# Kernel optimization log

Hardware: AMD Instinct MI355X
Metric: run time of the kernel (lower is better)

The kernel has to match this reference:

```python
import jax, jax.numpy as jnp
import numpy as np

HEADS = 8
DIM_HEAD = 64

def setup_inputs() -> dict:
    key = jax.random.key(0)
    ks = jax.random.split(key, 5)
    B, N, D = 2, 4096, 512  # query_dim = inner_dim = 512
    s = 0.02
    return {
        "x": jax.random.normal(ks[0], (B, N, D), dtype=jnp.float32),
        "Wq": jax.random.normal(ks[1], (D, D), dtype=jnp.float32) * s,
        "Wk": jax.random.normal(ks[2], (D, D), dtype=jnp.float32) * s,
        "Wv": jax.random.normal(ks[3], (D, D), dtype=jnp.float32) * s,
        "Wo": jax.random.normal(ks[4], (D, D), dtype=jnp.float32) * s,
        "bo": jnp.zeros((D,), dtype=jnp.float32),
    }

def reference(x, Wq, Wk, Wv, Wo, bo):
    B, N, D = x.shape
    h, dh = HEADS, DIM_HEAD
    scale = dh ** (-0.5)
    # self-attention: context = x
    q = x @ Wq  # [B, N, h*dh]
    k = x @ Wk
    v = x @ Wv
    # b n (h d) -> b h n d
    q = q.reshape(B, N, h, dh).transpose(0, 2, 1, 3)
    k = k.reshape(B, N, h, dh).transpose(0, 2, 1, 3)
    v = v.reshape(B, N, h, dh).transpose(0, 2, 1, 3)
    sim = jnp.einsum('bhid,bhjd->bhij', q, k) * scale  # full [B,h,N,N] matrix
    attn = jax.nn.softmax(sim, axis=-1)
    out = jnp.einsum('bhij,bhjd->bhid', attn, v)
    out = out.transpose(0, 2, 1, 3).reshape(B, N, h * dh)
    return out @ Wo + bo
```

## Files before the change

kernel.cpp:

```cpp
#include <hip/hip_runtime.h>
#include <hip/hip_bf16.h>
#include <stddef.h>
#include <stdint.h>

typedef __bf16 bf16_t;
typedef bf16_t bf16x8 __attribute__((ext_vector_type(8)));
typedef bf16_t bf16x4 __attribute__((ext_vector_type(4)));
typedef bf16_t bf16x2 __attribute__((ext_vector_type(2)));
typedef float floatx4 __attribute__((ext_vector_type(4)));
typedef float floatx16 __attribute__((ext_vector_type(16)));
typedef int   intx4  __attribute__((ext_vector_type(4)));

#define SEQ    4096
#define DMODEL 512
#define NH     8
#define BATCH  2
#define QSCALE 0.18033688011112042f

__device__ __forceinline__ void ld_lds16(const void* g, void* l) {
  __builtin_amdgcn_global_load_lds(
      (const __attribute__((address_space(1))) unsigned int*)g,
      (__attribute__((address_space(3))) unsigned int*)l, 16, 0, 0);
}

__global__ __launch_bounds__(256) void prep_k(
    const float* __restrict__ x,
    const float* __restrict__ W0, const float* __restrict__ W1,
    const float* __restrict__ W2, const float* __restrict__ W3,
    bf16_t* __restrict__ Wt, bf16_t* __restrict__ xb)
{
  if (blockIdx.z == 4) {
    const floatx4* xf = (const floatx4*)x;
    bf16x4* xo = (bf16x4*)xb;
    int base = (blockIdx.y * 16 + blockIdx.x) * 4096 + threadIdx.x;
    #pragma unroll
    for (int i = 0; i < 16; i++) {
      floatx4 v = xf[base + i * 256];
      xo[base + i * 256] = bf16x4{(bf16_t)v.x, (bf16_t)v.y, (bf16_t)v.z, (bf16_t)v.w};
    }
    return;
  }
  __shared__ float Ws[32][33];
  const float* W = (blockIdx.z == 0) ? W0 : (blockIdx.z == 1) ? W1
                 : (blockIdx.z == 2) ? W2 : W3;
  bf16_t* out = Wt + (size_t)blockIdx.z * DMODEL * DMODEL;
  const int tx = threadIdx.x & 31, ty = threadIdx.x >> 5;
  const int k0 = blockIdx.y * 32, n0 = blockIdx.x * 32;
  #pragma unroll
  for (int i = 0; i < 4; i++) {
    int kk = ty + i * 8;
    Ws[kk][tx] = W[(size_t)(k0 + kk) * DMODEL + n0 + tx];
  }
  __syncthreads();
  #pragma unroll
  for (int i = 0; i < 4; i++) {
    int nn = ty + i * 8;
    out[(size_t)(n0 + nn) * DMODEL + k0 + tx] = (bf16_t)Ws[tx][nn];
  }
}

__global__ __launch_bounds__(256) void qkv_k(
    const bf16_t* __restrict__ xb, const bf16_t* __restrict__ Wt,
    bf16_t* __restrict__ Qw, bf16_t* __restrict__ Ksw, bf16_t* __restrict__ Vsw)
{
  __shared__ __align__(16) char smem[2 * 1792 * 16];
  const int tid  = threadIdx.x;
  const int wave = tid >> 6;
  const int lane = tid & 63;
  const int lh   = lane >> 4, lm = lane & 15;
  const int bm   = blockIdx.x * 128;
  const int bn   = blockIdx.y * 32;

  int offA[4], ldsA[4];
  #pragma unroll
  for (int i = 0; i < 4; i++) {
    int S = i * 256 + wave * 64 + lane;
    int r = S >> 3, cc = (S & 7) ^ (r & 7);
    offA[i] = (bm + r) * DMODEL + cc * 8;
    ldsA[i] = (i * 256 + wave * 64) * 16;
  }
  int offB[3], ldsB[3];
  #pragma unroll
  for (int j = 0; j < 3; j++) {
    int S = j * 256 + wave * 64 + lane;
    int m = S >> 8, s2 = S & 255;
    int n = s2 >> 3, cc = (s2 & 7) ^ (n & 7);
    offB[j] = m * DMODEL * DMODEL + (bn + n) * DMODEL + cc * 8;
    ldsB[j] = (1024 + j * 256 + wave * 64) * 16;
  }

  floatx4 acc[3][2][2];
  #pragma unroll
  for (int m = 0; m < 3; m++)
    #pragma unroll
    for (int rb = 0; rb < 2; rb++)
      #pragma unroll
      for (int nb = 0; nb < 2; nb++)
        acc[m][rb][nb] = floatx4{0.f, 0.f, 0.f, 0.f};

  auto issue = [&](int kt, int buf) {
    char* bp = smem + buf * 1792 * 16;
    #pragma unroll
    for (int i = 0; i < 4; i++) ld_lds16(xb + offA[i] + kt * 64, bp + ldsA[i]);
    #pragma unroll
    for (int j = 0; j < 3; j++) ld_lds16(Wt + offB[j] + kt * 64, bp + ldsB[j]);
  };

  issue(0, 0);
  for (int kt = 0; kt < 8; kt++) {
    __syncthreads();
    if (kt < 7) issue(kt + 1, (kt + 1) & 1);
    const char* bp = smem + (kt & 1) * 1792 * 16;
    #pragma unroll
    for (int ks = 0; ks < 2; ks++) {
      int cc = ks * 4 + lh;
      int rA = wave * 32 + lm;
      bf16x8 a0 = *(const bf16x8*)(bp + (rA * 8 + (cc ^ (rA & 7))) * 16);
      bf16x8 a1 = *(const bf16x8*)(bp + ((rA + 16) * 8 + (cc ^ (rA & 7))) * 16);
      #pragma unroll
      for (int m = 0; m < 3; m++) {
        #pragma unroll
        for (int nb = 0; nb < 2; nb++) {
          int n = nb * 16 + lm;
          bf16x8 b = *(const bf16x8*)(bp + (1024 + m * 256 + n * 8 + (cc ^ (n & 7))) * 16);
          acc[m][0][nb] = __builtin_amdgcn_mfma_f32_16x16x32_bf16(a0, b, acc[m][0][nb], 0, 0, 0);
          acc[m][1][nb] = __builtin_amdgcn_mfma_f32_16x16x32_bf16(a1, b, acc[m][1][nb], 0, 0, 0);
        }
      }
    }
  }

  const int h  = bn >> 6;
  const int dl = bn & 63;
  #pragma unroll
  for (int rb = 0; rb < 2; rb++)
    #pragma unroll
    for (int nb = 0; nb < 2; nb++)
      #pragma unroll
      for (int r = 0; r < 4; r++) {
        int row = bm + wave * 32 + rb * 16 + lh * 4 + r;
        Qw[(size_t)row * DMODEL + bn + nb * 16 + lm] = (bf16_t)(acc[0][rb][nb][r] * QSCALE);
      }
  #pragma unroll
  for (int rb = 0; rb < 2; rb++)
    #pragma unroll
    for (int nb = 0; nb < 2; nb++) {
      int d = dl + nb * 16 + lm;
      #pragma unroll
      for (int r = 0; r < 4; r++) {
        int row = bm + wave * 32 + rb * 16 + lh * 4 + r;
        int bb = row >> 12, tk = row & 4095;
        size_t off = ((size_t)(bb * NH + h) * 64 + (tk >> 6)) * 4096
                   + (size_t)(tk & 63) * 64
                   + ((((d >> 3) ^ (tk & 7)) << 3) | (d & 7));
        Ksw[off] = (bf16_t)acc[1][rb][nb][r];
      }
    }
  bf16_t (*Ts)[136] = (bf16_t(*)[136])smem;
  __syncthreads();
  #pragma unroll
  for (int rb = 0; rb < 2; rb++)
    #pragma unroll
    for (int nb = 0; nb < 2; nb++) {
      int dloc = nb * 16 + lm, tok0 = wave * 32 + rb * 16 + lh * 4;
      bf16x4 v = {(bf16_t)acc[2][rb][nb][0], (bf16_t)acc[2][rb][nb][1],
                  (bf16_t)acc[2][rb][nb][2], (bf16_t)acc[2][rb][nb][3]};
      *(bf16x4*)&Ts[dloc][tok0] = v;
    }
  __syncthreads();
  {
    const int bb = bm >> 12, tk0 = bm & 4095;
    const size_t hb = (size_t)(bb * NH + h) * 64;
    #pragma unroll
    for (int i = 0; i < 2; i++) {
      int idx = tid + i * 256;
      int dloc = idx >> 4, c8 = idx & 15;
      int d = dl + dloc;
      bf16x8 val = *(bf16x8*)&Ts[dloc][c8 * 8];
      int cw = c8 & 7;
      int g = cw >> 1, sub = cw & 1;
      size_t tbase = (hb + (tk0 >> 6) + (c8 >> 3)) * 4096 + (size_t)d * 64;
      bf16x4 v0 = {val[0], val[1], val[2], val[3]};
      bf16x4 v1 = {val[4], val[5], val[6], val[7]};
      *(bf16x4*)&Vsw[tbase + (((2 * g) ^ (d & 7)) << 3) + sub * 4] = v0;
      *(bf16x4*)&Vsw[tbase + (((2 * g + 1) ^ (d & 7)) << 3) + sub * 4] = v1;
    }
  }
}

__global__ __launch_bounds__(256) void out_k(
    const bf16_t* __restrict__ A, const bf16_t* __restrict__ Wt,
    const float* __restrict__ bias, float* __restrict__ out)
{
  __shared__ __align__(16) char smem[2 * 1536 * 16];
  const int tid  = threadIdx.x;
  const int wave = tid >> 6;
  const int lane = tid & 63;
  const int lh   = lane >> 4, lm = lane & 15;
  const int bm   = blockIdx.x * 128;
  const int bn   = blockIdx.y * 64;

  int offA[4], ldsA[4];
  #pragma unroll
  for (int i = 0; i < 4; i++) {
    int S = i * 256 + wave * 64 + lane;
    int r = S >> 3, cc = (S & 7) ^ (r & 7);
    offA[i] = (bm + r) * DMODEL + cc * 8;
    ldsA[i] = (i * 256 + wave * 64) * 16;
  }
  int offB[2], ldsB[2];
  #pragma unroll
  for (int j = 0; j < 2; j++) {
    int S = j * 256 + wave * 64 + lane;
    int n = S >> 3, cc = (S & 7) ^ (n & 7);
    offB[j] = (bn + n) * DMODEL + cc * 8;
    ldsB[j] = (1024 + j * 256 + wave * 64) * 16;
  }

  floatx4 acc[2][4];
  #pragma unroll
  for (int rb = 0; rb < 2; rb++)
    #pragma unroll
    for (int nb = 0; nb < 4; nb++) acc[rb][nb] = floatx4{0.f, 0.f, 0.f, 0.f};

  auto issue = [&](int kt, int buf) {
    char* bp = smem + buf * 1536 * 16;
    #pragma unroll
    for (int i = 0; i < 4; i++) ld_lds16(A + offA[i] + kt * 64, bp + ldsA[i]);
    #pragma unroll
    for (int j = 0; j < 2; j++) ld_lds16(Wt + offB[j] + kt * 64, bp + ldsB[j]);
  };

  issue(0, 0);
  for (int kt = 0; kt < 8; kt++) {
    __syncthreads();
    if (kt < 7) issue(kt + 1, (kt + 1) & 1);
    const char* bp = smem + (kt & 1) * 1536 * 16;
    #pragma unroll
    for (int ks = 0; ks < 2; ks++) {
      int cc = ks * 4 + lh;
      int rA = wave * 32 + lm;
      bf16x8 a0 = *(const bf16x8*)(bp + (rA * 8 + (cc ^ (rA & 7))) * 16);
      bf16x8 a1 = *(const bf16x8*)(bp + ((rA + 16) * 8 + (cc ^ (rA & 7))) * 16);
      #pragma unroll
      for (int nb = 0; nb < 4; nb++) {
        int n = nb * 16 + lm;
        bf16x8 b = *(const bf16x8*)(bp + (1024 + n * 8 + (cc ^ (n & 7))) * 16);
        acc[0][nb] = __builtin_amdgcn_mfma_f32_16x16x32_bf16(a0, b, acc[0][nb], 0, 0, 0);
        acc[1][nb] = __builtin_amdgcn_mfma_f32_16x16x32_bf16(a1, b, acc[1][nb], 0, 0, 0);
      }
    }
  }

  #pragma unroll
  for (int rb = 0; rb < 2; rb++)
    #pragma unroll
    for (int nb = 0; nb < 4; nb++) {
      float bv = bias[bn + nb * 16 + lm];
      #pragma unroll
      for (int r = 0; r < 4; r++) {
        int row = bm + wave * 32 + rb * 16 + lh * 4 + r;
        out[(size_t)row * DMODEL + bn + nb * 16 + lm] = acc[rb][nb][r] + bv;
      }
    }
}

__global__ __launch_bounds__(512, 4) void attn_k(
    const bf16_t* __restrict__ Qw, const bf16_t* __restrict__ Ksw,
    const bf16_t* __restrict__ Vsw, bf16_t* __restrict__ Ow)
{
  __shared__ __align__(16) char smem[2 * 32768];
  const int tid  = threadIdx.x;
  const int wave = tid >> 6;
  const int qh   = wave >> 1;
  const int kh   = wave & 1;
  const int lane = tid & 63;
  const int hi   = lane >> 5;
  const int lo   = lane & 31;
  const int bh   = blockIdx.y, b = bh >> 3, h = bh & 7;
  const int q0   = blockIdx.x * 128;
  const size_t kvbase = (size_t)bh * 64 * 4096;

  const int qrow_g = b * SEQ + q0 + qh * 32 + lo;
  bf16x8 qreg[4];
  #pragma unroll
  for (int i = 0; i < 4; i++)
    qreg[i] = *(const bf16x8*)&Qw[(size_t)qrow_g * DMODEL + h * 64 + i * 16 + hi * 8];

  floatx16 accO[2];
  #pragma unroll
  for (int nbo = 0; nbo < 2; nbo++)
    #pragma unroll
    for (int j = 0; j < 16; j++) accO[nbo][j] = 0.f;
  float ls = 0.f;

  auto issue = [&](int s, int buf) {
    char* bp = smem + buf * 32768;
    const bf16_t* k0 = Ksw + kvbase + (size_t)(2 * s) * 4096;
    const bf16_t* v0 = Vsw + kvbase + (size_t)(2 * s) * 4096;
    ld_lds16(k0 + tid * 8,        bp + tid * 16);
    ld_lds16(v0 + tid * 8,        bp + 8192 + tid * 16);
    ld_lds16(k0 + 4096 + tid * 8, bp + 16384 + tid * 16);
    ld_lds16(v0 + 4096 + tid * 8, bp + 24576 + tid * 16);
  };

  issue(0, 0);
  for (int s = 0; s < SEQ / 128; s++) {
    __syncthreads();
    if (s < SEQ / 128 - 1) issue(s + 1, (s + 1) & 1);
    const bf16_t* Kb = (const bf16_t*)(smem + (s & 1) * 32768 + kh * 16384);
    const bf16_t* Vb = Kb + 4096;

    floatx16 accS[2];
    #pragma unroll
    for (int nb = 0; nb < 2; nb++)
      #pragma unroll
      for (int j = 0; j < 16; j++) accS[nb][j] = 0.f;
    #pragma unroll
    for (int kd = 0; kd < 4; kd++) {
      #pragma unroll
      for (int nb = 0; nb < 2; nb++) {
        int row = nb * 32 + lo;
        bf16x8 ak = *(const bf16x8*)&Kb[row * 64 + (((kd * 2 + hi) ^ (row & 7)) << 3)];
        accS[nb] = __builtin_amdgcn_mfma_f32_32x32x16_bf16(ak, qreg[kd], accS[nb], 0, 0, 0);
      }
    }

    int pk[2][8];
    #pragma unroll
    for (int nb = 0; nb < 2; nb++) {
      float p[16];
      #pragma unroll
      for (int r = 0; r < 16; r++) p[r] = __builtin_amdgcn_exp2f(accS[nb][r]);
      #pragma unroll
      for (int r = 0; r < 16; r += 4)
        ls += (p[r] + p[r + 1]) + (p[r + 2] + p[r + 3]);
      #pragma unroll
      for (int i = 0; i < 8; i++) {
        bf16x2 t2 = {(bf16_t)p[2 * i], (bf16_t)p[2 * i + 1]};
        pk[nb][i] = __builtin_bit_cast(int, t2);
      }
    }

    #pragma unroll
    for (int c = 0; c < 4; c++) {
      intx4 pi = {pk[c >> 1][4 * (c & 1)],     pk[c >> 1][4 * (c & 1) + 1],
                  pk[c >> 1][4 * (c & 1) + 2], pk[c >> 1][4 * (c & 1) + 3]};
      bf16x8 pf = __builtin_bit_cast(bf16x8, pi);
      #pragma unroll
      for (int nbo = 0; nbo < 2; nbo++) {
        int row = nbo * 32 + lo;
        bf16x8 av = *(const bf16x8*)&Vb[row * 64 + (((c * 2 + hi) ^ (row & 7)) << 3)];
        accO[nbo] = __builtin_amdgcn_mfma_f32_32x32x16_bf16(av, pf, accO[nbo], 0, 0, 0);
      }
    }
  }

  ls += __shfl_xor(ls, 32, 64);
  __syncthreads();
  float* mrg = (float*)smem;
  if (kh == 1) {
    #pragma unroll
    for (int nbo = 0; nbo < 2; nbo++) {
      float* dst = mrg + qh * 2720 + nbo * 1360 + lane * 20;
      #pragma unroll
      for (int g = 0; g < 4; g++) {
        dst[4 * g + 0] = accO[nbo][4 * g + 0];
        dst[4 * g + 1] = accO[nbo][4 * g + 1];
        dst[4 * g + 2] = accO[nbo][4 * g + 2];
        dst[4 * g + 3] = accO[nbo][4 * g + 3];
      }
    }
    if (hi == 0) mrg[10816 + qh * 32 + lo] = ls;
  }
  __syncthreads();
  if (kh == 0) {
    float linv = 1.0f / (ls + mrg[10816 + qh * 32 + lo]);
    #pragma unroll
    for (int nbo = 0; nbo < 2; nbo++) {
      const float* src = mrg + qh * 2720 + nbo * 1360 + lane * 20;
      #pragma unroll
      for (int g = 0; g < 4; g++) {
        accO[nbo][4 * g + 0] += src[4 * g + 0];
        accO[nbo][4 * g + 1] += src[4 * g + 1];
        accO[nbo][4 * g + 2] += src[4 * g + 2];
        accO[nbo][4 * g + 3] += src[4 * g + 3];
      }
    }
    bf16_t* Os = (bf16_t*)(smem + 49152 + qh * 4096);
    #pragma unroll
    for (int nbo = 0; nbo < 2; nbo++)
      #pragma unroll
      for (int g = 0; g < 4; g++) {
        int dbase = g * 8 + 4 * hi + 32 * nbo;
        bf16x4 v4 = {(bf16_t)(accO[nbo][4 * g] * linv),
                     (bf16_t)(accO[nbo][4 * g + 1] * linv),
                     (bf16_t)(accO[nbo][4 * g + 2] * linv),
                     (bf16_t)(accO[nbo][4 * g + 3] * linv)};
        *(bf16x4*)&Os[lo * 64 + (dbase ^ ((lo & 7) << 3))] = v4;
      }
    #pragma unroll
    for (int i = 0; i < 4; i++) {
      int idx = i * 64 + lane;
      int q = idx >> 3, c8 = idx & 7;
      bf16x8 v = *(const bf16x8*)&Os[q * 64 + ((c8 ^ (q & 7)) << 3)];
      int row_g = b * SEQ + q0 + qh * 32 + q;
      *(bf16x8*)&Ow[(size_t)row_g * DMODEL + h * 64 + c8 * 8] = v;
    }
  }
}

extern "C" void kernel_launch(void* const* d_in, const int* in_sizes, int n_in,
                              void* d_out, int out_size, void* d_ws, size_t ws_size,
                              hipStream_t stream)
{
  const float* x  = (const float*)d_in[0];
  const float* Wq = (const float*)d_in[1];
  const float* Wk = (const float*)d_in[2];
  const float* Wv = (const float*)d_in[3];
  const float* Wo = (const float*)d_in[4];
  const float* bo = (const float*)d_in[5];
  float* out = (float*)d_out;

  const int M = BATCH * SEQ;
  const size_t WT = (size_t)DMODEL * DMODEL;
  const size_t E  = (size_t)M * DMODEL;
  if (ws_size < (4 * WT + 3 * E) * sizeof(bf16_t)) return;

  bf16_t* Wt  = (bf16_t*)d_ws;
  bf16_t* Qw  = Wt + 4 * WT;
  bf16_t* Ksw = Qw + E;
  bf16_t* Vsw = Ksw + E;
  bf16_t* Ow  = Qw;
  bf16_t* xbf = (bf16_t*)d_out;

  prep_k<<<dim3(16, 16, 5), 256, 0, stream>>>(x, Wq, Wk, Wv, Wo, Wt, xbf);

  qkv_k<<<dim3(M / 128, DMODEL / 32), 256, 0, stream>>>(xbf, Wt, Qw, Ksw, Vsw);

  attn_k<<<dim3(SEQ / 128, BATCH * NH), 512, 0, stream>>>(Qw, Ksw, Vsw, Ow);

  out_k<<<dim3(M / 128, DMODEL / 64), 256, 0, stream>>>(Ow, Wt + 3 * WT, bo, out);
}
```

Baseline: 172.3 us.

## Use 512-thread blocks in projection GEMMs and compute softmax row sums via MFMA

The QKV and output projection kernels move from 256 to 512 threads per block, with each wave now owning 16 rows instead of 32. This gives more waves per block and halves each thread's accumulator and load work, but each B fragment read from LDS now feeds only one MFMA instead of two. In the attention kernel, the scalar accumulation of exp values into the row sum is replaced by an extra MFMA against a vector of ones, moving that reduction onto the matrix units. The ones-MFMA adds matrix work per step, and because it sums the bf16-rounded probabilities the normalizer now matches the values used in the PV product.

```diff
diff --git a/kernel.cpp b/kernel.cpp
--- a/kernel.cpp
+++ b/kernel.cpp
@@ -59,7 +59,7 @@
   }
 }
 
-__global__ __launch_bounds__(256) void qkv_k(
+__global__ __launch_bounds__(512) void qkv_k(
     const bf16_t* __restrict__ xb, const bf16_t* __restrict__ Wt,
     bf16_t* __restrict__ Qw, bf16_t* __restrict__ Ksw, bf16_t* __restrict__ Vsw)
 {
@@ -70,61 +70,61 @@
   const int lh   = lane >> 4, lm = lane & 15;
   const int bm   = blockIdx.x * 128;
   const int bn   = blockIdx.y * 32;
-
-  int offA[4], ldsA[4];
-  #pragma unroll
-  for (int i = 0; i < 4; i++) {
-    int S = i * 256 + wave * 64 + lane;
+  const int WT   = DMODEL * DMODEL;
+
+  int offA[2], ldsA[2];
+  #pragma unroll
+  for (int i = 0; i < 2; i++) {
+    int S = i * 512 + tid;
     int r = S >> 3, cc = (S & 7) ^ (r & 7);
     offA[i] = (bm + r) * DMODEL + cc * 8;
-    ldsA[i] = (i * 256 + wave * 64) * 16;
-  }
-  int offB[3], ldsB[3];
-  #pragma unroll
-  for (int j = 0; j < 3; j++) {
-    int S = j * 256 + wave * 64 + lane;
+    ldsA[i] = (i * 512 + wave * 64) * 16;
+  }
+  int offB[2], ldsB[2];
+  {
+    int S = tid;
     int m = S >> 8, s2 = S & 255;
     int n = s2 >> 3, cc = (s2 & 7) ^ (n & 7);
-    offB[j] = m * DMODEL * DMODEL + (bn + n) * DMODEL + cc * 8;
-    ldsB[j] = (1024 + j * 256 + wave * 64) * 16;
-  }
-
-  floatx4 acc[3][2][2];
+    offB[0] = m * WT + (bn + n) * DMODEL + cc * 8;
+    ldsB[0] = (1024 + wave * 64) * 16;
+    int S1 = 512 + tid;
+    int s21 = S1 & 255;
+    int n1 = s21 >> 3, cc1 = (s21 & 7) ^ (n1 & 7);
+    offB[1] = 2 * WT + (bn + n1) * DMODEL + cc1 * 8;
+    ldsB[1] = (1536 + wave * 64) * 16;
+  }
+
+  floatx4 acc[3][2];
   #pragma unroll
   for (int m = 0; m < 3; m++)
     #pragma unroll
-    for (int rb = 0; rb < 2; rb++)
-      #pragma unroll
-      for (int nb = 0; nb < 2; nb++)
-        acc[m][rb][nb] = floatx4{0.f, 0.f, 0.f, 0.f};
+    for (int nb = 0; nb < 2; nb++) acc[m][nb] = floatx4{0.f, 0.f, 0.f, 0.f};
 
   auto issue = [&](int kt, int buf) {
-    char* bp = smem + buf * 1792 * 16;
-    #pragma unroll
-    for (int i = 0; i < 4; i++) ld_lds16(xb + offA[i] + kt * 64, bp + ldsA[i]);
-    #pragma unroll
-    for (int j = 0; j < 3; j++) ld_lds16(Wt + offB[j] + kt * 64, bp + ldsB[j]);
+    char* bp = smem + buf * 28672;
+    ld_lds16(xb + offA[0] + kt * 64, bp + ldsA[0]);
+    ld_lds16(xb + offA[1] + kt * 64, bp + ldsA[1]);
+    ld_lds16(Wt + offB[0] + kt * 64, bp + ldsB[0]);
+    if (tid < 256) ld_lds16(Wt + offB[1] + kt * 64, bp + ldsB[1]);
   };
 
   issue(0, 0);
   for (int kt = 0; kt < 8; kt++) {
     __syncthreads();
     if (kt < 7) issue(kt + 1, (kt + 1) & 1);
-    const char* bp = smem + (kt & 1) * 1792 * 16;
+    const char* bp = smem + (kt & 1) * 28672;
+    int rA = wave * 16 + lm;
     #pragma unroll
     for (int ks = 0; ks < 2; ks++) {
       int cc = ks * 4 + lh;
-      int rA = wave * 32 + lm;
       bf16x8 a0 = *(const bf16x8*)(bp + (rA * 8 + (cc ^ (rA & 7))) * 16);
-      bf16x8 a1 = *(const bf16x8*)(bp + ((rA + 16) * 8 + (cc ^ (rA & 7))) * 16);
       #pragma unroll
       for (int m = 0; m < 3; m++) {
         #pragma unroll
         for (int nb = 0; nb < 2; nb++) {
           int n = nb * 16 + lm;
           bf16x8 b = *(const bf16x8*)(bp + (1024 + m * 256 + n * 8 + (cc ^ (n & 7))) * 16);
-          acc[m][0][nb] = __builtin_amdgcn_mfma_f32_16x16x32_bf16(a0, b, acc[m][0][nb], 0, 0, 0);
-          acc[m][1][nb] = __builtin_amdgcn_mfma_f32_16x16x32_bf16(a1, b, acc[m][1][nb], 0, 0, 0);
+          acc[m][nb] = __builtin_amdgcn_mfma_f32_16x16x32_bf16(a0, b, acc[m][nb], 0, 0, 0);
         }
       }
     }
@@ -133,62 +133,53 @@
   const int h  = bn >> 6;
   const int dl = bn & 63;
   #pragma unroll
-  for (int rb = 0; rb < 2; rb++)
-    #pragma unroll
-    for (int nb = 0; nb < 2; nb++)
-      #pragma unroll
-      for (int r = 0; r < 4; r++) {
-        int row = bm + wave * 32 + rb * 16 + lh * 4 + r;
-        Qw[(size_t)row * DMODEL + bn + nb * 16 + lm] = (bf16_t)(acc[0][rb][nb][r] * QSCALE);
-      }
-  #pragma unroll
-  for (int rb = 0; rb < 2; rb++)
-    #pragma unroll
-    for (int nb = 0; nb < 2; nb++) {
-      int d = dl + nb * 16 + lm;
-      #pragma unroll
-      for (int r = 0; r < 4; r++) {
-        int row = bm + wave * 32 + rb * 16 + lh * 4 + r;
-        int bb = row >> 12, tk = row & 4095;
-        size_t off = ((size_t)(bb * NH + h) * 64 + (tk >> 6)) * 4096
-                   + (size_t)(tk & 63) * 64
-                   + ((((d >> 3) ^ (tk & 7)) << 3) | (d & 7));
-        Ksw[off] = (bf16_t)acc[1][rb][nb][r];
-      }
-    }
+  for (int nb = 0; nb < 2; nb++)
+    #pragma unroll
+    for (int r = 0; r < 4; r++) {
+      int row = bm + wave * 16 + lh * 4 + r;
+      Qw[(size_t)row * DMODEL + bn + nb * 16 + lm] = (bf16_t)(acc[0][nb][r] * QSCALE);
+    }
+  #pragma unroll
+  for (int nb = 0; nb < 2; nb++) {
+    int d = dl + nb * 16 + lm;
+    #pragma unroll
+    for (int r = 0; r < 4; r++) {
+      int row = bm + wave * 16 + lh * 4 + r;
+      int bb = row >> 12, tk = row & 4095;
+      size_t off = ((size_t)(bb * NH + h) * 64 + (tk >> 6)) * 4096
+                 + (size_t)(tk & 63) * 64
+                 + ((((d >> 3) ^ (tk & 7)) << 3) | (d & 7));
+      Ksw[off] = (bf16_t)acc[1][nb][r];
+    }
+  }
   bf16_t (*Ts)[136] = (bf16_t(*)[136])smem;
   __syncthreads();
   #pragma unroll
-  for (int rb = 0; rb < 2; rb++)
-    #pragma unroll
-    for (int nb = 0; nb < 2; nb++) {
-      int dloc = nb * 16 + lm, tok0 = wave * 32 + rb * 16 + lh * 4;
-      bf16x4 v = {(bf16_t)acc[2][rb][nb][0], (bf16_t)acc[2][rb][nb][1],
-                  (bf16_t)acc[2][rb][nb][2], (bf16_t)acc[2][rb][nb][3]};
-      *(bf16x4*)&Ts[dloc][tok0] = v;
-    }
+  for (int nb = 0; nb < 2; nb++) {
+    int dloc = nb * 16 + lm, tok0 = wave * 16 + lh * 4;
+    bf16x4 v = {(bf16_t)acc[2][nb][0], (bf16_t)acc[2][nb][1],
+                (bf16_t)acc[2][nb][2], (bf16_t)acc[2][nb][3]};
+    *(bf16x4*)&Ts[dloc][tok0] = v;
+  }
   __syncthreads();
   {
     const int bb = bm >> 12, tk0 = bm & 4095;
     const size_t hb = (size_t)(bb * NH + h) * 64;
-    #pragma unroll
-    for (int i = 0; i < 2; i++) {
-      int idx = tid + i * 256;
-      int dloc = idx >> 4, c8 = idx & 15;
-      int d = dl + dloc;
-      bf16x8 val = *(bf16x8*)&Ts[dloc][c8 * 8];
-      int cw = c8 & 7;
-      int g = cw >> 1, sub = cw & 1;
-      size_t tbase = (hb + (tk0 >> 6) + (c8 >> 3)) * 4096 + (size_t)d * 64;
-      bf16x4 v0 = {val[0], val[1], val[2], val[3]};
-      bf16x4 v1 = {val[4], val[5], val[6], val[7]};
-      *(bf16x4*)&Vsw[tbase + (((2 * g) ^ (d & 7)) << 3) + sub * 4] = v0;
-      *(bf16x4*)&Vsw[tbase + (((2 * g + 1) ^ (d & 7)) << 3) + sub * 4] = v1;
-    }
-  }
-}
-
-__global__ __launch_bounds__(256) void out_k(
+    int idx = tid;
+    int dloc = idx >> 4, c8 = idx & 15;
+    int d = dl + dloc;
+    bf16x8 val = *(bf16x8*)&Ts[dloc][c8 * 8];
+    int cw = c8 & 7;
+    int g = cw >> 1, sub = cw & 1;
+    size_t tbase = (hb + (tk0 >> 6) + (c8 >> 3)) * 4096 + (size_t)d * 64;
+    bf16x4 v0 = {val[0], val[1], val[2], val[3]};
+    bf16x4 v1 = {val[4], val[5], val[6], val[7]};
+    *(bf16x4*)&Vsw[tbase + (((2 * g) ^ (d & 7)) << 3) + sub * 4] = v0;
+    *(bf16x4*)&Vsw[tbase + (((2 * g + 1) ^ (d & 7)) << 3) + sub * 4] = v1;
+  }
+}
+
+__global__ __launch_bounds__(512) void out_k(
     const bf16_t* __restrict__ A, const bf16_t* __restrict__ Wt,
     const float* __restrict__ bias, float* __restrict__ out)
 {
@@ -200,69 +191,61 @@
   const int bm   = blockIdx.x * 128;
   const int bn   = blockIdx.y * 64;
 
-  int offA[4], ldsA[4];
-  #pragma unroll
-  for (int i = 0; i < 4; i++) {
-    int S = i * 256 + wave * 64 + lane;
+  int offA[2], ldsA[2];
+  #pragma unroll
+  for (int i = 0; i < 2; i++) {
+    int S = i * 512 + tid;
     int r = S >> 3, cc = (S & 7) ^ (r & 7);
     offA[i] = (bm + r) * DMODEL + cc * 8;
-    ldsA[i] = (i * 256 + wave * 64) * 16;
-  }
-  int offB[2], ldsB[2];
-  #pragma unroll
-  for (int j = 0; j < 2; j++) {
-    int S = j * 256 + wave * 64 + lane;
+    ldsA[i] = (i * 512 + wave * 64) * 16;
+  }
+  int offB, ldsOB;
+  {
+    int S = tid;
     int n = S >> 3, cc = (S & 7) ^ (n & 7);
-    offB[j] = (bn + n) * DMODEL + cc * 8;
-    ldsB[j] = (1024 + j * 256 + wave * 64) * 16;
-  }
-
-  floatx4 acc[2][4];
-  #pragma unroll
-  for (int rb = 0; rb < 2; rb++)
-    #pragma unroll
-    for (int nb = 0; nb < 4; nb++) acc[rb][nb] = floatx4{0.f, 0.f, 0.f, 0.f};
+    offB  = (bn + n) * DMODEL + cc * 8;
+    ldsOB = (1024 + wave * 64) * 16;
+  }
+
+  floatx4 acc[4];
+  #pragma unroll
+  for (int nb = 0; nb < 4; nb++) acc[nb] = floatx4{0.f, 0.f, 0.f, 0.f};
 
   auto issue = [&](int kt, int buf) {
-    char* bp = smem + buf * 1536 * 16;
-    #pragma unroll
-    for (int i = 0; i < 4; i++) ld_lds16(A + offA[i] + kt * 64, bp + ldsA[i]);
-    #pragma unroll
-    for (int j = 0; j < 2; j++) ld_lds16(Wt + offB[j] + kt * 64, bp + ldsB[j]);
+    char* bp = smem + buf * 24576;
+    ld_lds16(A + offA[0] + kt * 64, bp + ldsA[0]);
+    ld_lds16(A + offA[1] + kt * 64, bp + ldsA[1]);
+    ld_lds16(Wt + offB + kt * 64, bp + ldsOB);
   };
 
   issue(0, 0);
   for (int kt = 0; kt < 8; kt++) {
     __syncthreads();
     if (kt < 7) issue(kt + 1, (kt + 1) & 1);
-    const char* bp = smem + (kt & 1) * 1536 * 16;
+    const char* bp = smem + (kt & 1) * 24576;
+    int rA = wave * 16 + lm;
     #pragma unroll
     for (int ks = 0; ks < 2; ks++) {
       int cc = ks * 4 + lh;
-      int rA = wave * 32 + lm;
       bf16x8 a0 = *(const bf16x8*)(bp + (rA * 8 + (cc ^ (rA & 7))) * 16);
-      bf16x8 a1 = *(const bf16x8*)(bp + ((rA + 16) * 8 + (cc ^ (rA & 7))) * 16);
       #pragma unroll
       for (int nb = 0; nb < 4; nb++) {
         int n = nb * 16 + lm;
         bf16x8 b = *(const bf16x8*)(bp + (1024 + n * 8 + (cc ^ (n & 7))) * 16);
-        acc[0][nb] = __builtin_amdgcn_mfma_f32_16x16x32_bf16(a0, b, acc[0][nb], 0, 0, 0);
-        acc[1][nb] = __builtin_amdgcn_mfma_f32_16x16x32_bf16(a1, b, acc[1][nb], 0, 0, 0);
-      }
-    }
-  }
-
-  #pragma unroll
-  for (int rb = 0; rb < 2; rb++)
-    #pragma unroll
-    for (int nb = 0; nb < 4; nb++) {
-      float bv = bias[bn + nb * 16 + lm];
-      #pragma unroll
-      for (int r = 0; r < 4; r++) {
-        int row = bm + wave * 32 + rb * 16 + lh * 4 + r;
-        out[(size_t)row * DMODEL + bn + nb * 16 + lm] = acc[rb][nb][r] + bv;
-      }
-    }
+        acc[nb] = __builtin_amdgcn_mfma_f32_16x16x32_bf16(a0, b, acc[nb], 0, 0, 0);
+      }
+    }
+  }
+
+  #pragma unroll
+  for (int nb = 0; nb < 4; nb++) {
+    float bv = bias[bn + nb * 16 + lm];
+    #pragma unroll
+    for (int r = 0; r < 4; r++) {
+      int row = bm + wave * 16 + lh * 4 + r;
+      out[(size_t)row * DMODEL + bn + nb * 16 + lm] = acc[nb][r] + bv;
+    }
+  }
 }
 
 __global__ __launch_bounds__(512, 4) void attn_k(
@@ -287,12 +270,17 @@
   for (int i = 0; i < 4; i++)
     qreg[i] = *(const bf16x8*)&Qw[(size_t)qrow_g * DMODEL + h * 64 + i * 16 + hi * 8];
 
-  floatx16 accO[2];
+  bf16x8 ones;
+  #pragma unroll
+  for (int i = 0; i < 8; i++) ones[i] = (bf16_t)1.0f;
+
+  floatx16 accO[2], accL;
   #pragma unroll
   for (int nbo = 0; nbo < 2; nbo++)
     #pragma unroll
     for (int j = 0; j < 16; j++) accO[nbo][j] = 0.f;
-  float ls = 0.f;
+  #pragma unroll
+  for (int j = 0; j < 16; j++) accL[j] = 0.f;
 
   auto issue = [&](int s, int buf) {
     char* bp = smem + buf * 32768;
@@ -333,9 +321,6 @@
       #pragma unroll
       for (int r = 0; r < 16; r++) p[r] = __builtin_amdgcn_exp2f(accS[nb][r]);
       #pragma unroll
-      for (int r = 0; r < 16; r += 4)
-        ls += (p[r] + p[r + 1]) + (p[r + 2] + p[r + 3]);
-      #pragma unroll
       for (int i = 0; i < 8; i++) {
         bf16x2 t2 = {(bf16_t)p[2 * i], (bf16_t)p[2 * i + 1]};
         pk[nb][i] = __builtin_bit_cast(int, t2);
@@ -347,6 +332,7 @@
       intx4 pi = {pk[c >> 1][4 * (c & 1)],     pk[c >> 1][4 * (c & 1) + 1],
                   pk[c >> 1][4 * (c & 1) + 2], pk[c >> 1][4 * (c & 1) + 3]};
       bf16x8 pf = __builtin_bit_cast(bf16x8, pi);
+      accL = __builtin_amdgcn_mfma_f32_32x32x16_bf16(ones, pf, accL, 0, 0, 0);
       #pragma unroll
       for (int nbo = 0; nbo < 2; nbo++) {
         int row = nbo * 32 + lo;
@@ -356,7 +342,7 @@
     }
   }
 
-  ls += __shfl_xor(ls, 32, 64);
+  float ls = accL[0];
   __syncthreads();
   float* mrg = (float*)smem;
   if (kh == 1) {
@@ -436,9 +422,9 @@
 
   prep_k<<<dim3(16, 16, 5), 256, 0, stream>>>(x, Wq, Wk, Wv, Wo, Wt, xbf);
 
-  qkv_k<<<dim3(M / 128, DMODEL / 32), 256, 0, stream>>>(xbf, Wt, Qw, Ksw, Vsw);
+  qkv_k<<<dim3(M / 128, DMODEL / 32), 512, 0, stream>>>(xbf, Wt, Qw, Ksw, Vsw);
 
   attn_k<<<dim3(SEQ / 128, BATCH * NH), 512, 0, stream>>>(Qw, Ksw, Vsw, Ow);
 
-  out_k<<<dim3(M / 128, DMODEL / 64), 256, 0, stream>>>(Ow, Wt + 3 * WT, bo, out);
-}
+  out_k<<<dim3(M / 128, DMODEL / 64), 512, 0, stream>>>(Ow, Wt + 3 * WT, bo, out);
+}
```

Result: no change. 175.1 us (+1.6%).

## Double row tiles in QKV and attention kernels to reuse weight and K/V loads

Applied to the files above, without the earlier changes.

The QKV projection kernel now covers 256 rows per block in two 128-row halves with separate A and B buffers, so each weight tile is loaded once for twice as many rows. The attention kernel moves to 1024 threads per block covering 256 queries, so each K/V tile staged in LDS serves twice as many query rows. The cross-wave accumulator merge is reorganised to fit LDS, at the cost of extra barriers. The larger blocks halve the grid and add register pressure per thread, which can lower occupancy.

```diff
diff --git a/kernel.cpp b/kernel.cpp
--- a/kernel.cpp
+++ b/kernel.cpp
@@ -63,68 +63,77 @@
     const bf16_t* __restrict__ xb, const bf16_t* __restrict__ Wt,
     bf16_t* __restrict__ Qw, bf16_t* __restrict__ Ksw, bf16_t* __restrict__ Vsw)
 {
-  __shared__ __align__(16) char smem[2 * 1792 * 16];
+  __shared__ __align__(16) char smem[57344];
   const int tid  = threadIdx.x;
   const int wave = tid >> 6;
   const int lane = tid & 63;
   const int lh   = lane >> 4, lm = lane & 15;
-  const int bm   = blockIdx.x * 128;
+  const int bm0  = blockIdx.x * 256;
   const int bn   = blockIdx.y * 32;
-
-  int offA[4], ldsA[4];
+  const int WTsz = DMODEL * DMODEL;
+
+  int offAr[4], ldsA[4];
   #pragma unroll
   for (int i = 0; i < 4; i++) {
-    int S = i * 256 + wave * 64 + lane;
+    int S = i * 256 + tid;
     int r = S >> 3, cc = (S & 7) ^ (r & 7);
-    offA[i] = (bm + r) * DMODEL + cc * 8;
+    offAr[i] = r * DMODEL + cc * 8;
     ldsA[i] = (i * 256 + wave * 64) * 16;
   }
   int offB[3], ldsB[3];
   #pragma unroll
   for (int j = 0; j < 3; j++) {
-    int S = j * 256 + wave * 64 + lane;
-    int m = S >> 8, s2 = S & 255;
+    int s2 = tid;
     int n = s2 >> 3, cc = (s2 & 7) ^ (n & 7);
-    offB[j] = m * DMODEL * DMODEL + (bn + n) * DMODEL + cc * 8;
-    ldsB[j] = (1024 + j * 256 + wave * 64) * 16;
-  }
-
-  floatx4 acc[3][2][2];
-  #pragma unroll
-  for (int m = 0; m < 3; m++)
-    #pragma unroll
-    for (int rb = 0; rb < 2; rb++)
-      #pragma unroll
-      for (int nb = 0; nb < 2; nb++)
-        acc[m][rb][nb] = floatx4{0.f, 0.f, 0.f, 0.f};
-
-  auto issue = [&](int kt, int buf) {
-    char* bp = smem + buf * 1792 * 16;
-    #pragma unroll
-    for (int i = 0; i < 4; i++) ld_lds16(xb + offA[i] + kt * 64, bp + ldsA[i]);
+    offB[j] = j * WTsz + (bn + n) * DMODEL + cc * 8;
+    ldsB[j] = (j * 256 + wave * 64) * 16;
+  }
+
+  floatx4 acc[2][3][2][2];
+  #pragma unroll
+  for (int mh = 0; mh < 2; mh++)
+    #pragma unroll
+    for (int m = 0; m < 3; m++)
+      #pragma unroll
+      for (int rb = 0; rb < 2; rb++)
+        #pragma unroll
+        for (int nb = 0; nb < 2; nb++)
+          acc[mh][m][rb][nb] = floatx4{0.f, 0.f, 0.f, 0.f};
+
+  auto issueA = [&](int it) {
+    int kt = it >> 1, mh = it & 1;
+    char* bp = smem + (it & 1) * 16384;
+    const bf16_t* base = xb + (size_t)(bm0 + mh * 128) * DMODEL + kt * 64;
+    #pragma unroll
+    for (int i = 0; i < 4; i++) ld_lds16(base + offAr[i], bp + ldsA[i]);
+  };
+  auto issueB = [&](int kt) {
+    char* bp = smem + 32768 + (kt & 1) * 12288;
     #pragma unroll
     for (int j = 0; j < 3; j++) ld_lds16(Wt + offB[j] + kt * 64, bp + ldsB[j]);
   };
 
-  issue(0, 0);
-  for (int kt = 0; kt < 8; kt++) {
+  issueA(0); issueB(0);
+  for (int j = 0; j < 16; j++) {
     __syncthreads();
-    if (kt < 7) issue(kt + 1, (kt + 1) & 1);
-    const char* bp = smem + (kt & 1) * 1792 * 16;
+    if (j < 15) { issueA(j + 1); if (j & 1) issueB((j + 1) >> 1); }
+    const char* bpA = smem + (j & 1) * 16384;
+    const char* bpB = smem + 32768 + ((j >> 1) & 1) * 12288;
+    const int mh = j & 1;
+    int rA = wave * 32 + lm;
     #pragma unroll
     for (int ks = 0; ks < 2; ks++) {
       int cc = ks * 4 + lh;
-      int rA = wave * 32 + lm;
-      bf16x8 a0 = *(const bf16x8*)(bp + (rA * 8 + (cc ^ (rA & 7))) * 16);
-      bf16x8 a1 = *(const bf16x8*)(bp + ((rA + 16) * 8 + (cc ^ (rA & 7))) * 16);
+      bf16x8 a0 = *(const bf16x8*)(bpA + (rA * 8 + (cc ^ (rA & 7))) * 16);
+      bf16x8 a1 = *(const bf16x8*)(bpA + ((rA + 16) * 8 + (cc ^ (rA & 7))) * 16);
       #pragma unroll
       for (int m = 0; m < 3; m++) {
         #pragma unroll
         for (int nb = 0; nb < 2; nb++) {
           int n = nb * 16 + lm;
-          bf16x8 b = *(const bf16x8*)(bp + (1024 + m * 256 + n * 8 + (cc ^ (n & 7))) * 16);
-          acc[m][0][nb] = __builtin_amdgcn_mfma_f32_16x16x32_bf16(a0, b, acc[m][0][nb], 0, 0, 0);
-          acc[m][1][nb] = __builtin_amdgcn_mfma_f32_16x16x32_bf16(a1, b, acc[m][1][nb], 0, 0, 0);
+          bf16x8 b = *(const bf16x8*)(bpB + (m * 256 + n * 8 + (cc ^ (n & 7))) * 16);
+          acc[mh][m][0][nb] = __builtin_amdgcn_mfma_f32_16x16x32_bf16(a0, b, acc[mh][m][0][nb], 0, 0, 0);
+          acc[mh][m][1][nb] = __builtin_amdgcn_mfma_f32_16x16x32_bf16(a1, b, acc[mh][m][1][nb], 0, 0, 0);
         }
       }
     }
@@ -133,43 +142,45 @@
   const int h  = bn >> 6;
   const int dl = bn & 63;
   #pragma unroll
-  for (int rb = 0; rb < 2; rb++)
-    #pragma unroll
-    for (int nb = 0; nb < 2; nb++)
-      #pragma unroll
-      for (int r = 0; r < 4; r++) {
-        int row = bm + wave * 32 + rb * 16 + lh * 4 + r;
-        Qw[(size_t)row * DMODEL + bn + nb * 16 + lm] = (bf16_t)(acc[0][rb][nb][r] * QSCALE);
-      }
-  #pragma unroll
-  for (int rb = 0; rb < 2; rb++)
-    #pragma unroll
-    for (int nb = 0; nb < 2; nb++) {
-      int d = dl + nb * 16 + lm;
-      #pragma unroll
-      for (int r = 0; r < 4; r++) {
-        int row = bm + wave * 32 + rb * 16 + lh * 4 + r;
-        int bb = row >> 12, tk = row & 4095;
-        size_t off = ((size_t)(bb * NH + h) * 64 + (tk >> 6)) * 4096
-                   + (size_t)(tk & 63) * 64
-                   + ((((d >> 3) ^ (tk & 7)) << 3) | (d & 7));
-        Ksw[off] = (bf16_t)acc[1][rb][nb][r];
-      }
-    }
-  bf16_t (*Ts)[136] = (bf16_t(*)[136])smem;
-  __syncthreads();
-  #pragma unroll
-  for (int rb = 0; rb < 2; rb++)
-    #pragma unroll
-    for (int nb = 0; nb < 2; nb++) {
-      int dloc = nb * 16 + lm, tok0 = wave * 32 + rb * 16 + lh * 4;
-      bf16x4 v = {(bf16_t)acc[2][rb][nb][0], (bf16_t)acc[2][rb][nb][1],
-                  (bf16_t)acc[2][rb][nb][2], (bf16_t)acc[2][rb][nb][3]};
-      *(bf16x4*)&Ts[dloc][tok0] = v;
-    }
-  __syncthreads();
-  {
-    const int bb = bm >> 12, tk0 = bm & 4095;
+  for (int mh = 0; mh < 2; mh++) {
+    #pragma unroll
+    for (int rb = 0; rb < 2; rb++)
+      #pragma unroll
+      for (int nb = 0; nb < 2; nb++) {
+        int row = bm0 + mh * 128 + wave * 32 + rb * 16 + lh * 4;
+        int d = dl + nb * 16 + lm;
+        #pragma unroll
+        for (int r = 0; r < 4; r++) {
+          Qw[(size_t)(row + r) * DMODEL + bn + nb * 16 + lm] =
+              (bf16_t)(acc[mh][0][rb][nb][r] * QSCALE);
+          int rw = row + r, bb = rw >> 12, tk = rw & 4095;
+          size_t off = ((size_t)(bb * NH + h) * 64 + (tk >> 6)) * 4096
+                     + (size_t)(tk & 63) * 64
+                     + ((((d >> 3) ^ (tk & 7)) << 3) | (d & 7));
+          Ksw[off] = (bf16_t)acc[mh][1][rb][nb][r];
+        }
+      }
+  }
+  __syncthreads();
+  #pragma unroll
+  for (int mh = 0; mh < 2; mh++) {
+    bf16_t (*Ts)[136] = (bf16_t(*)[136])(smem + mh * 16384);
+    #pragma unroll
+    for (int rb = 0; rb < 2; rb++)
+      #pragma unroll
+      for (int nb = 0; nb < 2; nb++) {
+        int dloc = nb * 16 + lm, tok0 = wave * 32 + rb * 16 + lh * 4;
+        bf16x4 v = {(bf16_t)acc[mh][2][rb][nb][0], (bf16_t)acc[mh][2][rb][nb][1],
+                    (bf16_t)acc[mh][2][rb][nb][2], (bf16_t)acc[mh][2][rb][nb][3]};
+        *(bf16x4*)&Ts[dloc][tok0] = v;
+      }
+  }
+  __syncthreads();
+  #pragma unroll
+  for (int mh = 0; mh < 2; mh++) {
+    bf16_t (*Ts)[136] = (bf16_t(*)[136])(smem + mh * 16384);
+    const int bmh = bm0 + mh * 128;
+    const int bb = bmh >> 12, tk0 = bmh & 4095;
     const size_t hb = (size_t)(bb * NH + h) * 64;
     #pragma unroll
     for (int i = 0; i < 2; i++) {
@@ -265,7 +276,7 @@
     }
 }
 
-__global__ __launch_bounds__(512, 4) void attn_k(
+__global__ __launch_bounds__(1024, 4) void attn_k(
     const bf16_t* __restrict__ Qw, const bf16_t* __restrict__ Ksw,
     const bf16_t* __restrict__ Vsw, bf16_t* __restrict__ Ow)
 {
@@ -278,7 +289,7 @@
   const int hi   = lane >> 5;
   const int lo   = lane & 31;
   const int bh   = blockIdx.y, b = bh >> 3, h = bh & 7;
-  const int q0   = blockIdx.x * 128;
+  const int q0   = blockIdx.x * 256;
   const size_t kvbase = (size_t)bh * 64 * 4096;
 
   const int qrow_g = b * SEQ + q0 + qh * 32 + lo;
@@ -298,10 +309,11 @@
     char* bp = smem + buf * 32768;
     const bf16_t* k0 = Ksw + kvbase + (size_t)(2 * s) * 4096;
     const bf16_t* v0 = Vsw + kvbase + (size_t)(2 * s) * 4096;
-    ld_lds16(k0 + tid * 8,        bp + tid * 16);
-    ld_lds16(v0 + tid * 8,        bp + 8192 + tid * 16);
-    ld_lds16(k0 + 4096 + tid * 8, bp + 16384 + tid * 16);
-    ld_lds16(v0 + 4096 + tid * 8, bp + 24576 + tid * 16);
+    const bf16_t* sA = (tid < 512) ? (k0 + tid * 8) : (v0 + (tid - 512) * 8);
+    ld_lds16(sA, bp + tid * 16);
+    const bf16_t* sB = (tid < 512) ? (k0 + 4096 + tid * 8)
+                                   : (v0 + 4096 + (tid - 512) * 8);
+    ld_lds16(sB, bp + 16384 + tid * 16);
   };
 
   issue(0, 0);
@@ -358,11 +370,17 @@
 
   ls += __shfl_xor(ls, 32, 64);
   __syncthreads();
-  float* mrg = (float*)smem;
-  if (kh == 1) {
-    #pragma unroll
-    for (int nbo = 0; nbo < 2; nbo++) {
-      float* dst = mrg + qh * 2720 + nbo * 1360 + lane * 20;
+  float* lsx = (float*)smem;
+  if (kh == 1 && hi == 0) lsx[qh * 32 + lo] = ls;
+  __syncthreads();
+  float linv = 0.f;
+  if (kh == 0) linv = 1.0f / (ls + lsx[qh * 32 + lo]);
+  float* mrg = (float*)smem + 1024;
+  #pragma unroll
+  for (int nbo = 0; nbo < 2; nbo++) {
+    __syncthreads();
+    if (kh == 1) {
+      float* dst = mrg + qh * 1360 + lane * 20;
       #pragma unroll
       for (int g = 0; g < 4; g++) {
         dst[4 * g + 0] = accO[nbo][4 * g + 0];
@@ -371,14 +389,9 @@
         dst[4 * g + 3] = accO[nbo][4 * g + 3];
       }
     }
-    if (hi == 0) mrg[10816 + qh * 32 + lo] = ls;
-  }
-  __syncthreads();
-  if (kh == 0) {
-    float linv = 1.0f / (ls + mrg[10816 + qh * 32 + lo]);
-    #pragma unroll
-    for (int nbo = 0; nbo < 2; nbo++) {
-      const float* src = mrg + qh * 2720 + nbo * 1360 + lane * 20;
+    __syncthreads();
+    if (kh == 0) {
+      const float* src = mrg + qh * 1360 + lane * 20;
       #pragma unroll
       for (int g = 0; g < 4; g++) {
         accO[nbo][4 * g + 0] += src[4 * g + 0];
@@ -387,7 +400,10 @@
         accO[nbo][4 * g + 3] += src[4 * g + 3];
       }
     }
-    bf16_t* Os = (bf16_t*)(smem + 49152 + qh * 4096);
+  }
+  __syncthreads();
+  if (kh == 0) {
+    bf16_t* Os = (bf16_t*)(smem) + qh * 2048;
     #pragma unroll
     for (int nbo = 0; nbo < 2; nbo++)
       #pragma unroll
@@ -436,9 +452,9 @@
 
   prep_k<<<dim3(16, 16, 5), 256, 0, stream>>>(x, Wq, Wk, Wv, Wo, Wt, xbf);
 
-  qkv_k<<<dim3(M / 128, DMODEL / 32), 256, 0, stream>>>(xbf, Wt, Qw, Ksw, Vsw);
-
-  attn_k<<<dim3(SEQ / 128, BATCH * NH), 512, 0, stream>>>(Qw, Ksw, Vsw, Ow);
+  qkv_k<<<dim3(M / 256, DMODEL / 32), 256, 0, stream>>>(xbf, Wt, Qw, Ksw, Vsw);
+
+  attn_k<<<dim3(SEQ / 256, BATCH * NH), 1024, 0, stream>>>(Qw, Ksw, Vsw, Ow);
 
   out_k<<<dim3(M / 128, DMODEL / 64), 256, 0, stream>>>(Ow, Wt + 3 * WT, bo, out);
 }
```

Result: no change. 173.5 us (+0.7%).
